# Kernel tuning notes

Hardware: AMD Instinct MI355X
Metric: run time of the kernel (lower is better)

## Reference

```python
import jax, jax.numpy as jnp
import numpy as np

B, S, D_MODEL, D_QK, D_VO = 4, 2048, 1024, 128, 128
NEG = -1.0e9


def setup_inputs() -> dict:
    key = jax.random.key(0)
    k1, k2, k3, k4, k5 = jax.random.split(key, 5)
    enc = jax.random.normal(k1, (B, S, D_MODEL), dtype=jnp.float32)
    # causal mask: True means masked (masked_fill), broadcast over batch
    causal = jnp.triu(jnp.ones((S, S), dtype=bool), k=1)
    mask = jnp.broadcast_to(causal, (B, S, S))
    scale = 0.02
    W_q = jax.random.normal(k2, (D_MODEL, D_QK), dtype=jnp.float32) * scale
    W_k = jax.random.normal(k3, (D_MODEL, D_QK), dtype=jnp.float32) * scale
    W_v = jax.random.normal(k4, (D_MODEL, D_VO), dtype=jnp.float32) * scale
    W_o = jax.random.normal(k5, (D_VO, D_MODEL), dtype=jnp.float32) * scale
    return {"encodings": enc, "mask": mask, "W_q": W_q, "W_k": W_k, "W_v": W_v, "W_o": W_o}


def reference(encodings, mask, W_q, W_k, W_v, W_o):
    # q,k: [B,S,d_qk]; v: [B,S,d_vo]
    q = jnp.einsum('bsd,de->bse', encodings, W_q)
    k = jnp.einsum('bsd,de->bse', encodings, W_k)
    v = jnp.einsum('bsd,de->bse', encodings, W_v)
    sims = jnp.einsum('bqe,bke->bqk', q, k) / jnp.asarray(D_QK ** 0.5, q.dtype)
    sims = jnp.where(mask, jnp.asarray(NEG, sims.dtype), sims)
    attn = jax.nn.softmax(sims, axis=-1)  # [B,S,S]
    scores = jnp.einsum('bqk,bke->bqe', attn, v)  # [B,S,d_vo]
    return jnp.einsum('bse,ed->bsd', scores, W_o)  # [B,S,d_model]
```

## Files before the change

kernel.cpp:

```cpp
#include <hip/hip_runtime.h>
#include <hip/hip_bf16.h>
#include <stdint.h>

typedef __attribute__((ext_vector_type(8))) short short8;
typedef __attribute__((ext_vector_type(4))) float floatx4;

using bf16 = __hip_bfloat16;

#define SCALE_L2 0.12751793359133147f

__device__ inline unsigned short f2b(float f) {
    bf16 h = __float2bfloat16(f);
    return *(unsigned short*)&h;
}
__device__ inline float b2f(unsigned short u) {
    union { unsigned int i; float f; } v;
    v.i = ((unsigned int)u) << 16;
    return v.f;
}

__device__ __forceinline__ void gll16(const bf16* g, bf16* l) {
    __builtin_amdgcn_global_load_lds((__attribute__((address_space(1))) void*)g,
                                     (__attribute__((address_space(3))) void*)l,
                                     16, 0, 0);
}

__global__ __launch_bounds__(256) void prep_all(const float4* __restrict__ enc4,
                                                ushort4* __restrict__ encb4,
                                                const float* __restrict__ Wq,
                                                const float* __restrict__ Wk,
                                                const float* __restrict__ Wv,
                                                const float* __restrict__ Wo,
                                                bf16* __restrict__ Wqkvt,
                                                bf16* __restrict__ Wot) {
    int bx = blockIdx.x;
    if (bx < 8192) {
        int i = bx * 256 + threadIdx.x;
        float4 v = enc4[i];
        ushort4 o;
        o.x = f2b(v.x); o.y = f2b(v.y); o.z = f2b(v.z); o.w = f2b(v.w);
        encb4[i] = o;
    } else {
        int idx = (bx - 8192) * 256 + threadIdx.x;
        int sel = idx >> 17;
        int i = idx & 131071;
        if (sel < 3) {
            const float* W = (sel == 0) ? Wq : (sel == 1) ? Wk : Wv;
            int r = i >> 7, c = i & 127;
            Wqkvt[(size_t)(sel * 128 + c) * 1024 + r] = __float2bfloat16(W[i]);
        } else {
            int r = i >> 10, c = i & 1023;
            Wot[(size_t)c * 128 + r] = __float2bfloat16(Wo[i]);
        }
    }
}

__global__ __launch_bounds__(256) void gemm_qkv(const bf16* __restrict__ A,
                                                const bf16* __restrict__ Bt,
                                                bf16* __restrict__ Qb,
                                                bf16* __restrict__ Kb,
                                                bf16* __restrict__ Vtb) {
    __shared__ bf16 As[64 * 32];
    __shared__ bf16 Bs[128 * 32];

    const int tid = threadIdx.x;
    const int m0 = blockIdx.x * 64;
    const int nsel = blockIdx.y;
    const int brow0 = nsel * 128;
    const int w = tid >> 6, lane = tid & 63;
    const int wm = (w >> 1) * 32, wn = (w & 1) * 64;
    const int quad = lane >> 4, l16 = lane & 15;

    const int ar = tid >> 2, akq = (tid & 3) * 8;
    const int br1 = (tid + 256) >> 2;
    bf16* As_w  = &As[w * 512];
    bf16* Bs_w0 = &Bs[w * 512];
    bf16* Bs_w1 = &Bs[2048 + w * 512];

    floatx4 acc[2][4];
#pragma unroll
    for (int i = 0; i < 2; i++)
#pragma unroll
        for (int j = 0; j < 4; j++) acc[i][j] = (floatx4){0.f, 0.f, 0.f, 0.f};

    for (int k0 = 0; k0 < 1024; k0 += 32) {
        __syncthreads();
        gll16(&A[(size_t)(m0 + ar) * 1024 + k0 + akq], As_w);
        gll16(&Bt[(size_t)(brow0 + ar) * 1024 + k0 + akq], Bs_w0);
        gll16(&Bt[(size_t)(brow0 + br1) * 1024 + k0 + akq], Bs_w1);
        __syncthreads();

        short8 a[2], b[4];
#pragma unroll
        for (int mt = 0; mt < 2; mt++)
            a[mt] = *(const short8*)&As[(wm + mt * 16 + l16) * 32 + quad * 8];
#pragma unroll
        for (int nt = 0; nt < 4; nt++)
            b[nt] = *(const short8*)&Bs[(wn + nt * 16 + l16) * 32 + quad * 8];
#pragma unroll
        for (int mt = 0; mt < 2; mt++)
#pragma unroll
            for (int nt = 0; nt < 4; nt++)
                acc[mt][nt] = __builtin_amdgcn_mfma_f32_16x16x32_bf16(a[mt], b[nt], acc[mt][nt], 0, 0, 0);
    }

#pragma unroll
    for (int mt = 0; mt < 2; mt++)
#pragma unroll
        for (int nt = 0; nt < 4; nt++)
#pragma unroll
            for (int r = 0; r < 4; r++) {
                int row = m0 + wm + mt * 16 + quad * 4 + r;
                int col = wn + nt * 16 + l16;
                bf16 h = __float2bfloat16(acc[mt][nt][r]);
                if (nsel == 0) {
                    Qb[(size_t)row * 128 + col] = h;
                } else if (nsel == 1) {
                    Kb[(size_t)row * 128 + col] = h;
                } else {
                    int bb = row >> 11, ss = row & 2047;
                    Vtb[(size_t)bb * 262144 + (size_t)col * 2048 + ss] = h;
                }
            }
}

__global__ __launch_bounds__(256) void gemm_out(const bf16* __restrict__ A,
                                                const bf16* __restrict__ Bt,
                                                float* __restrict__ C) {
    __shared__ bf16 As[64 * 40];
    __shared__ bf16 Bs[128 * 40];

    const int tid = threadIdx.x;
    const int m0 = blockIdx.x * 64;
    const int n0 = blockIdx.y * 128;
    const int w = tid >> 6, lane = tid & 63;
    const int wm = (w >> 1) * 32, wn = (w & 1) * 64;
    const int quad = lane >> 4, l16 = lane & 15;

    const int ra = tid >> 2, ca = (tid & 3) * 8;
    const int rb0 = tid >> 2, rb1 = (tid + 256) >> 2;

    floatx4 acc[2][4];
#pragma unroll
    for (int i = 0; i < 2; i++)
#pragma unroll
        for (int j = 0; j < 4; j++) acc[i][j] = (floatx4){0.f, 0.f, 0.f, 0.f};

    int4 pa  = *(const int4*)&A[(size_t)(m0 + ra) * 128 + ca];
    int4 pb0 = *(const int4*)&Bt[(size_t)(n0 + rb0) * 128 + ca];
    int4 pb1 = *(const int4*)&Bt[(size_t)(n0 + rb1) * 128 + ca];

    for (int k0 = 0; k0 < 128; k0 += 32) {
        __syncthreads();
        *(int4*)&As[ra * 40 + ca] = pa;
        *(int4*)&Bs[rb0 * 40 + ca] = pb0;
        *(int4*)&Bs[rb1 * 40 + ca] = pb1;
        __syncthreads();

        if (k0 + 32 < 128) {
            pa  = *(const int4*)&A[(size_t)(m0 + ra) * 128 + k0 + 32 + ca];
            pb0 = *(const int4*)&Bt[(size_t)(n0 + rb0) * 128 + k0 + 32 + ca];
            pb1 = *(const int4*)&Bt[(size_t)(n0 + rb1) * 128 + k0 + 32 + ca];
        }

        short8 a[2], b[4];
#pragma unroll
        for (int mt = 0; mt < 2; mt++)
            a[mt] = *(const short8*)&As[(wm + mt * 16 + l16) * 40 + quad * 8];
#pragma unroll
        for (int nt = 0; nt < 4; nt++)
            b[nt] = *(const short8*)&Bs[(wn + nt * 16 + l16) * 40 + quad * 8];
#pragma unroll
        for (int mt = 0; mt < 2; mt++)
#pragma unroll
            for (int nt = 0; nt < 4; nt++)
                acc[mt][nt] = __builtin_amdgcn_mfma_f32_16x16x32_bf16(a[mt], b[nt], acc[mt][nt], 0, 0, 0);
    }

#pragma unroll
    for (int mt = 0; mt < 2; mt++)
#pragma unroll
        for (int nt = 0; nt < 4; nt++)
#pragma unroll
            for (int r = 0; r < 4; r++) {
                int row = m0 + wm + mt * 16 + quad * 4 + r;
                int col = n0 + wn + nt * 16 + l16;
                C[(size_t)row * 1024 + col] = acc[mt][nt][r];
            }
}

__global__ __launch_bounds__(256) void flash_split(const bf16* __restrict__ Q,
                                                   const bf16* __restrict__ K,
                                                   const bf16* __restrict__ Vt,
                                                   bf16* __restrict__ Opb,
                                                   float2* __restrict__ Ml) {
    __shared__ bf16 Ks[64 * 136];
    __shared__ bf16 Vs[128 * 72];
    __shared__ bf16 Ps[4 * 16 * 72];

    const int tid = threadIdx.x;
    const int x = blockIdx.x;
    const int b = x / 144;
    const int id = x - b * 144;
    const int g = (id >= 112) ? 7 : (id >= 84) ? 6 : (id >= 60) ? 5 : (id >= 40) ? 4
                : (id >= 24) ? 3 : (id >= 12) ? 2 : (id >= 4) ? 1 : 0;
    const int nc = g + 1;
    const int local = id - 2 * g * nc;
    const int qi = local / nc;
    const int c = local - qi * nc;
    const int qt = 4 * g + qi;
    const int q0 = qt * 64;
    const int start = 4 * c;
    const int end = min(start + 4, qt + 1);

    const int w = tid >> 6, lane = tid & 63;
    const int quad = lane >> 4, l16 = lane & 15;

    const int qrow = q0 + w * 16 + l16;
    const bf16* Qrow = &Q[((size_t)b * 2048 + qrow) * 128];
    short8 qf[4];
#pragma unroll
    for (int k4 = 0; k4 < 4; k4++)
        qf[k4] = *(const short8*)&Qrow[k4 * 32 + quad * 8];

    float m_run = -1.0e30f, l_run = 0.f;
    floatx4 o[8];
#pragma unroll
    for (int d = 0; d < 8; d++) o[d] = (floatx4){0.f, 0.f, 0.f, 0.f};

    int4 kreg[4], vreg[4];
    const int sr[4]  = {(tid + 0) >> 4, (tid + 256) >> 4, (tid + 512) >> 4, (tid + 768) >> 4};
    const int scg    = (tid & 15) * 8;
    const int sr2[4] = {(tid + 0) >> 3, (tid + 256) >> 3, (tid + 512) >> 3, (tid + 768) >> 3};
    const int scg2   = (tid & 7) * 8;

#pragma unroll
    for (int i = 0; i < 4; i++) {
        kreg[i] = *(const int4*)&K[((size_t)b * 2048 + start * 64 + sr[i]) * 128 + scg];
        vreg[i] = *(const int4*)&Vt[(size_t)b * 262144 + (size_t)sr2[i] * 2048 + start * 64 + scg2];
    }

    for (int kt = start; kt < end; kt++) {
        __syncthreads();
#pragma unroll
        for (int i = 0; i < 4; i++) {
            *(int4*)&Ks[sr[i] * 136 + scg] = kreg[i];
            *(int4*)&Vs[sr2[i] * 72 + scg2] = vreg[i];
        }
        __syncthreads();

        if (kt + 1 < end) {
#pragma unroll
            for (int i = 0; i < 4; i++) {
                kreg[i] = *(const int4*)&K[((size_t)b * 2048 + (kt + 1) * 64 + sr[i]) * 128 + scg];
                vreg[i] = *(const int4*)&Vt[(size_t)b * 262144 + (size_t)sr2[i] * 2048 + (kt + 1) * 64 + scg2];
            }
        }

        floatx4 s_acc[4];
#pragma unroll
        for (int nt = 0; nt < 4; nt++) {
            s_acc[nt] = (floatx4){0.f, 0.f, 0.f, 0.f};
#pragma unroll
            for (int k4 = 0; k4 < 4; k4++) {
                short8 kf = *(const short8*)&Ks[(nt * 16 + l16) * 136 + k4 * 32 + quad * 8];
                s_acc[nt] = __builtin_amdgcn_mfma_f32_16x16x32_bf16(kf, qf[k4], s_acc[nt], 0, 0, 0);
            }
        }

        float sv[4][4];
#pragma unroll
        for (int nt = 0; nt < 4; nt++)
#pragma unroll
            for (int r = 0; r < 4; r++) {
                float s = s_acc[nt][r] * SCALE_L2;
                if (kt == qt) {
                    int kcol = kt * 64 + nt * 16 + quad * 4 + r;
                    if (kcol > qrow) s = -1.0e9f;
                }
                sv[nt][r] = s;
            }

        float t0 = fmaxf(fmaxf(sv[0][0], sv[0][1]), fmaxf(sv[0][2], sv[0][3]));
        float t1 = fmaxf(fmaxf(sv[1][0], sv[1][1]), fmaxf(sv[1][2], sv[1][3]));
        float t2 = fmaxf(fmaxf(sv[2][0], sv[2][1]), fmaxf(sv[2][2], sv[2][3]));
        float t3 = fmaxf(fmaxf(sv[3][0], sv[3][1]), fmaxf(sv[3][2], sv[3][3]));
        float tmax = fmaxf(fmaxf(t0, t1), fmaxf(t2, t3));
        tmax = fmaxf(tmax, __shfl_xor(tmax, 16));
        tmax = fmaxf(tmax, __shfl_xor(tmax, 32));

        float mnew = fmaxf(m_run, tmax);
        float alpha = exp2f(m_run - mnew);
        m_run = mnew;

        float rsum = 0.f;
#pragma unroll
        for (int nt = 0; nt < 4; nt++)
#pragma unroll
            for (int r = 0; r < 4; r++) {
                float p = exp2f(sv[nt][r] - mnew);
                sv[nt][r] = p;
                rsum += p;
            }
        rsum += __shfl_xor(rsum, 16);
        rsum += __shfl_xor(rsum, 32);
        l_run = l_run * alpha + rsum;

#pragma unroll
        for (int nt = 0; nt < 4; nt++) {
            ushort4 pk;
            pk.x = f2b(sv[nt][0]); pk.y = f2b(sv[nt][1]);
            pk.z = f2b(sv[nt][2]); pk.w = f2b(sv[nt][3]);
            *(ushort4*)&Ps[w * 1152 + l16 * 72 + nt * 16 + quad * 4] = pk;
        }

#pragma unroll
        for (int d = 0; d < 8; d++) {
            o[d][0] *= alpha; o[d][1] *= alpha; o[d][2] *= alpha; o[d][3] *= alpha;
        }

        short8 pf[2];
#pragma unroll
        for (int k2 = 0; k2 < 2; k2++)
            pf[k2] = *(const short8*)&Ps[w * 1152 + l16 * 72 + k2 * 32 + quad * 8];
#pragma unroll
        for (int d = 0; d < 8; d++)
#pragma unroll
            for (int k2 = 0; k2 < 2; k2++) {
                short8 vf = *(const short8*)&Vs[(d * 16 + l16) * 72 + k2 * 32 + quad * 8];
                o[d] = __builtin_amdgcn_mfma_f32_16x16x32_bf16(vf, pf[k2], o[d], 0, 0, 0);
            }
    }

    const int lrow = w * 16 + l16;
    const size_t obase = ((size_t)x * 64 + lrow) * 128;
#pragma unroll
    for (int d = 0; d < 8; d++) {
        ushort4 pk;
        pk.x = f2b(o[d][0]); pk.y = f2b(o[d][1]);
        pk.z = f2b(o[d][2]); pk.w = f2b(o[d][3]);
        *(ushort4*)&Opb[obase + d * 16 + quad * 4] = pk;
    }
    if (lane < 16) Ml[(size_t)x * 64 + lrow] = make_float2(m_run, l_run);
}

__global__ __launch_bounds__(256) void flash_merge(const bf16* __restrict__ Opb,
                                                   const float2* __restrict__ Ml,
                                                   bf16* __restrict__ Sc) {
    int idx = blockIdx.x * 256 + threadIdx.x;
    int row = idx >> 5, dg = (idx & 31) * 4;
    int b = row >> 11, s = row & 2047;
    int qt = s >> 6, rl = s & 63;
    int g = qt >> 2, nc = g + 1;
    int id0 = b * 144 + 2 * g * nc + (qt & 3) * nc;

    float m[8], l[8], M = -1.0e30f;
    for (int j = 0; j < nc; j++) {
        float2 t = Ml[(size_t)(id0 + j) * 64 + rl];
        m[j] = t.x; l[j] = t.y;
        M = fmaxf(M, t.x);
    }
    float L = 0.f;
    float a0 = 0.f, a1 = 0.f, a2 = 0.f, a3 = 0.f;
    for (int j = 0; j < nc; j++) {
        float wj = exp2f(m[j] - M);
        L += l[j] * wj;
        ushort4 p = *(const ushort4*)&Opb[((size_t)(id0 + j) * 64 + rl) * 128 + dg];
        a0 += wj * b2f(p.x); a1 += wj * b2f(p.y);
        a2 += wj * b2f(p.z); a3 += wj * b2f(p.w);
    }
    float inv = 1.0f / L;
    ushort4 o;
    o.x = f2b(a0 * inv); o.y = f2b(a1 * inv);
    o.z = f2b(a2 * inv); o.w = f2b(a3 * inv);
    *(ushort4*)&Sc[(size_t)row * 128 + dg] = o;
}

extern "C" void kernel_launch(void* const* d_in, const int* in_sizes, int n_in,
                              void* d_out, int out_size, void* d_ws, size_t ws_size,
                              hipStream_t stream) {
    const float* enc = (const float*)d_in[0];
    const float* Wq = (const float*)d_in[2];
    const float* Wk = (const float*)d_in[3];
    const float* Wv = (const float*)d_in[4];
    const float* Wo = (const float*)d_in[5];
    float* out = (float*)d_out;

    const size_t MB = 1024 * 1024;
    char* ws = (char*)d_ws;
    bf16*   encb  = (bf16*)(ws);
    bf16*   Opb   = (bf16*)(ws);
    bf16*   Qb    = (bf16*)(ws + 16 * MB);
    bf16*   Kb    = (bf16*)(ws + 18 * MB);
    bf16*   Vtb   = (bf16*)(ws + 20 * MB);
    bf16*   Scb   = (bf16*)(ws + 22 * MB);
    bf16*   Wqkvt = (bf16*)(ws + 24 * MB);
    bf16*   Wot   = (bf16*)(ws + 24 * MB + 768 * 1024);
    float2* Ml    = (float2*)(ws + 25 * MB);

    prep_all<<<10240, 256, 0, stream>>>((const float4*)enc, (ushort4*)encb,
                                        Wq, Wk, Wv, Wo, Wqkvt, Wot);

    dim3 blk(256);
    gemm_qkv<<<dim3(128, 3), blk, 0, stream>>>(encb, Wqkvt, Qb, Kb, Vtb);

    flash_split<<<576, blk, 0, stream>>>(Qb, Kb, Vtb, Opb, Ml);
    flash_merge<<<1024, blk, 0, stream>>>(Opb, Ml, Scb);

    gemm_out<<<dim3(128, 8), blk, 0, stream>>>(Scb, Wot, out);
}
```

Measured before the change: 211.4 us.

## Load K and V fragments directly from global memory, dropping shared staging

The flash split kernel stops staging K and V tiles through shared memory with block-wide barriers and register prefetch. Each wave now loads its MFMA operand fragments for K and V straight from global memory, which removes both __syncthreads per tile and shrinks LDS use to a per-wave P buffer. That buffer is reused to transpose the output so it can be written as coalesced 16-byte stores. The cost is that the four waves each reload the same K/V data, relying on the caches, and the loads are no longer prefetched a tile ahead.

```diff
diff --git a/kernel.cpp b/kernel.cpp
--- a/kernel.cpp
+++ b/kernel.cpp
@@ -194,9 +194,7 @@
                                                    const bf16* __restrict__ Vt,
                                                    bf16* __restrict__ Opb,
                                                    float2* __restrict__ Ml) {
-    __shared__ bf16 Ks[64 * 136];
-    __shared__ bf16 Vs[128 * 72];
-    __shared__ bf16 Ps[4 * 16 * 72];
+    __shared__ bf16 Pw[4 * 2176];
 
     const int tid = threadIdx.x;
     const int x = blockIdx.x;
@@ -215,6 +213,7 @@
 
     const int w = tid >> 6, lane = tid & 63;
     const int quad = lane >> 4, l16 = lane & 15;
+    bf16* myP = &Pw[w * 2176];
 
     const int qrow = q0 + w * 16 + l16;
     const bf16* Qrow = &Q[((size_t)b * 2048 + qrow) * 128];
@@ -223,49 +222,29 @@
     for (int k4 = 0; k4 < 4; k4++)
         qf[k4] = *(const short8*)&Qrow[k4 * 32 + quad * 8];
 
+    const bf16* Kl = &K[((size_t)b * 2048 + l16) * 128 + quad * 8];
+    const bf16* Vl = &Vt[(size_t)b * 262144 + (size_t)l16 * 2048 + quad * 8];
+
     float m_run = -1.0e30f, l_run = 0.f;
     floatx4 o[8];
 #pragma unroll
     for (int d = 0; d < 8; d++) o[d] = (floatx4){0.f, 0.f, 0.f, 0.f};
 
-    int4 kreg[4], vreg[4];
-    const int sr[4]  = {(tid + 0) >> 4, (tid + 256) >> 4, (tid + 512) >> 4, (tid + 768) >> 4};
-    const int scg    = (tid & 15) * 8;
-    const int sr2[4] = {(tid + 0) >> 3, (tid + 256) >> 3, (tid + 512) >> 3, (tid + 768) >> 3};
-    const int scg2   = (tid & 7) * 8;
-
-#pragma unroll
-    for (int i = 0; i < 4; i++) {
-        kreg[i] = *(const int4*)&K[((size_t)b * 2048 + start * 64 + sr[i]) * 128 + scg];
-        vreg[i] = *(const int4*)&Vt[(size_t)b * 262144 + (size_t)sr2[i] * 2048 + start * 64 + scg2];
-    }
-
     for (int kt = start; kt < end; kt++) {
-        __syncthreads();
-#pragma unroll
-        for (int i = 0; i < 4; i++) {
-            *(int4*)&Ks[sr[i] * 136 + scg] = kreg[i];
-            *(int4*)&Vs[sr2[i] * 72 + scg2] = vreg[i];
-        }
-        __syncthreads();
-
-        if (kt + 1 < end) {
-#pragma unroll
-            for (int i = 0; i < 4; i++) {
-                kreg[i] = *(const int4*)&K[((size_t)b * 2048 + (kt + 1) * 64 + sr[i]) * 128 + scg];
-                vreg[i] = *(const int4*)&Vt[(size_t)b * 262144 + (size_t)sr2[i] * 2048 + (kt + 1) * 64 + scg2];
-            }
-        }
+        short8 kc[16];
+#pragma unroll
+        for (int nt = 0; nt < 4; nt++)
+#pragma unroll
+            for (int k4 = 0; k4 < 4; k4++)
+                kc[nt * 4 + k4] = *(const short8*)&Kl[(size_t)(kt * 64 + nt * 16) * 128 + k4 * 32];
 
         floatx4 s_acc[4];
 #pragma unroll
         for (int nt = 0; nt < 4; nt++) {
             s_acc[nt] = (floatx4){0.f, 0.f, 0.f, 0.f};
 #pragma unroll
-            for (int k4 = 0; k4 < 4; k4++) {
-                short8 kf = *(const short8*)&Ks[(nt * 16 + l16) * 136 + k4 * 32 + quad * 8];
-                s_acc[nt] = __builtin_amdgcn_mfma_f32_16x16x32_bf16(kf, qf[k4], s_acc[nt], 0, 0, 0);
-            }
+            for (int k4 = 0; k4 < 4; k4++)
+                s_acc[nt] = __builtin_amdgcn_mfma_f32_16x16x32_bf16(kc[nt * 4 + k4], qf[k4], s_acc[nt], 0, 0, 0);
         }
 
         float sv[4][4];
@@ -311,7 +290,7 @@
             ushort4 pk;
             pk.x = f2b(sv[nt][0]); pk.y = f2b(sv[nt][1]);
             pk.z = f2b(sv[nt][2]); pk.w = f2b(sv[nt][3]);
-            *(ushort4*)&Ps[w * 1152 + l16 * 72 + nt * 16 + quad * 4] = pk;
+            *(ushort4*)&myP[l16 * 72 + nt * 16 + quad * 4] = pk;
         }
 
 #pragma unroll
@@ -322,26 +301,33 @@
         short8 pf[2];
 #pragma unroll
         for (int k2 = 0; k2 < 2; k2++)
-            pf[k2] = *(const short8*)&Ps[w * 1152 + l16 * 72 + k2 * 32 + quad * 8];
+            pf[k2] = *(const short8*)&myP[l16 * 72 + k2 * 32 + quad * 8];
 #pragma unroll
         for (int d = 0; d < 8; d++)
 #pragma unroll
             for (int k2 = 0; k2 < 2; k2++) {
-                short8 vf = *(const short8*)&Vs[(d * 16 + l16) * 72 + k2 * 32 + quad * 8];
+                short8 vf = *(const short8*)&Vl[(size_t)(d * 16) * 2048 + kt * 64 + k2 * 32];
                 o[d] = __builtin_amdgcn_mfma_f32_16x16x32_bf16(vf, pf[k2], o[d], 0, 0, 0);
             }
     }
 
-    const int lrow = w * 16 + l16;
-    const size_t obase = ((size_t)x * 64 + lrow) * 128;
 #pragma unroll
     for (int d = 0; d < 8; d++) {
         ushort4 pk;
         pk.x = f2b(o[d][0]); pk.y = f2b(o[d][1]);
         pk.z = f2b(o[d][2]); pk.w = f2b(o[d][3]);
-        *(ushort4*)&Opb[obase + d * 16 + quad * 4] = pk;
-    }
-    if (lane < 16) Ml[(size_t)x * 64 + lrow] = make_float2(m_run, l_run);
+        *(ushort4*)&myP[l16 * 136 + d * 16 + quad * 4] = pk;
+    }
+    const int er = lane >> 2;
+    const int ec = lane & 3;
+    const size_t orow = ((size_t)x * 64 + w * 16 + er) * 128;
+#pragma unroll
+    for (int p = 0; p < 4; p++) {
+        int ce = (p * 4 + ec) * 8;
+        short8 t = *(const short8*)&myP[er * 136 + ce];
+        *(short8*)&Opb[orow + ce] = t;
+    }
+    if (lane < 16) Ml[(size_t)x * 64 + w * 16 + l16] = make_float2(m_run, l_run);
 }
 
 __global__ __launch_bounds__(256) void flash_merge(const bf16* __restrict__ Opb,
```

New measurement: 213.7 us. No clear change (+1.1%).
